# Kernel tuning notes

Hardware: AMD Instinct MI355X
Metric: run time of the kernel (lower is better)

Reference implementation:

```python
import jax, jax.numpy as jnp
import numpy as np

B, D, T, H, OUT = 256, 256, 256, 512, 256

def setup_inputs() -> dict:
    key = jax.random.key(0)
    ks = jax.random.split(key, 7)
    s = lambda fan: 1.0 / np.sqrt(fan)
    x = jax.random.normal(ks[0], (B, D, T), dtype=jnp.float32)
    Wx = jax.random.normal(ks[1], (D, H), dtype=jnp.float32) * s(D)
    Wh = jax.random.normal(ks[2], (H, H), dtype=jnp.float32) * s(H)
    b = jnp.zeros((H,), dtype=jnp.float32)
    Wout = jax.random.normal(ks[3], (H, OUT), dtype=jnp.float32) * s(H)
    bout = jnp.zeros((OUT,), dtype=jnp.float32)
    init_state = jnp.zeros((1, H), dtype=jnp.float32)  # non-trainable zeros in keras
    return {"x": x, "Wx": Wx, "Wh": Wh, "b": b, "Wout": Wout, "bout": bout, "init_state": init_state}

def reference(x, Wx, Wh, b, Wout, bout, init_state):
    # x: [B, D, T] (time on last axis, as unstacked in the keras layer)
    batch = x.shape[0]
    h0 = jnp.tile(init_state, (batch, 1))              # [B, H]
    xs = jnp.moveaxis(x, -1, 0)                        # [T, B, D]
    # precompute input projections for all steps (hoisted out of the recurrence)
    xproj = jnp.einsum('tbd,dh->tbh', xs, Wx) + b      # [T, B, H]

    def step(h_prev, xp):
        cur = jnp.tanh(xp + h_prev @ Wh)
        # residual: state_i = cell_out + state_{i-1}; at i=0 h_prev is zeros, so always adding is exact
        new = cur + h_prev
        return new, new

    _, states = jax.lax.scan(step, h0, xproj)          # states: [T, B, H]
    states = jnp.moveaxis(states, 0, 1)                # [B, T, H]
    out = states @ Wout + bout                         # [B, T, OUT]
    return out
```

## Files before the change

### kernel.cpp

```cpp
#include <hip/hip_runtime.h>
#include <cstring>
#include <cstdio>

typedef __attribute__((ext_vector_type(8))) short short8;
typedef __attribute__((ext_vector_type(4))) float f32x4;
typedef __attribute__((ext_vector_type(4))) unsigned u32x4;

__device__ __forceinline__ short f2bf(float f){
  unsigned u; __builtin_memcpy(&u, &f, 4);
  u += 0x7FFFu + ((u >> 16) & 1u);
  return (short)(u >> 16);
}
__device__ __forceinline__ float bf2f(short s){
  unsigned u = ((unsigned)(unsigned short)s) << 16;
  float f; __builtin_memcpy(&f, &u, 4);
  return f;
}
__device__ __forceinline__ void split2(float v, short& hi, short& lo){
  hi = f2bf(v);
  float r = v - bf2f(hi);
  lo = f2bf(r);
}
__device__ __forceinline__ unsigned pack2(float v){
  short hi, lo; split2(v, hi, lo);
  return (((unsigned)(unsigned short)hi) << 16) | (unsigned)(unsigned short)lo;
}
__device__ __forceinline__ float tanh_fast(float x){
  float e = __expf(2.0f * x);
  return 1.0f - 2.0f / (e + 1.0f);
}

#define HIDX(r,k) ((((r) * 512) + (k)) ^ (((r) & 7) << 3))

__global__ void transpose_split(const float* __restrict__ in,
                                short* __restrict__ outh, short* __restrict__ outl,
                                int R, int C){
  int idx = blockIdx.x * 256 + threadIdx.x;
  if (idx < R * C){
    int r = idx / C, c = idx % C;
    short h, l; split2(in[(size_t)r * C + c], h, l);
    outh[(size_t)c * R + r] = h;
    outl[(size_t)c * R + r] = l;
  }
}

__global__ void transpose_to_bf16(const float* __restrict__ in, short* __restrict__ out,
                                  int R, int C){
  int idx = blockIdx.x * 256 + threadIdx.x;
  if (idx < R * C){
    int r = idx / C, c = idx % C;
    out[(size_t)c * R + r] = f2bf(in[(size_t)r * C + c]);
  }
}

__global__ __launch_bounds__(256) void transpose_x_split(const float* __restrict__ x,
                                                         short* __restrict__ xTh,
                                                         short* __restrict__ xTl){
  __shared__ float tile[64][65];
  const int b = blockIdx.x, d0 = blockIdx.y * 64, t0 = blockIdx.z * 64;
  const int tid = threadIdx.x;
  const float* xp = x + ((size_t)b * 256 + d0) * 256 + t0;
  for (int v = tid; v < 1024; v += 256){
    int r = v >> 4, c4 = (v & 15) * 4;
    float4 f = *(const float4*)(xp + (size_t)r * 256 + c4);
    tile[r][c4+0] = f.x; tile[r][c4+1] = f.y; tile[r][c4+2] = f.z; tile[r][c4+3] = f.w;
  }
  __syncthreads();
  for (int v = tid; v < 512; v += 256){
    int j = v >> 3, i8 = (v & 7) * 8;
    short8 oh, ol;
    #pragma unroll
    for (int u = 0; u < 8; ++u){ short h, l; split2(tile[i8 + u][j], h, l); oh[u] = h; ol[u] = l; }
    size_t off = ((size_t)(t0 + j) * 256 + b) * 256 + d0 + i8;
    *(short8*)(xTh + off) = oh;
    *(short8*)(xTl + off) = ol;
  }
}

__global__ __launch_bounds__(256) void gemm1_split(
    const short* __restrict__ Ah, const short* __restrict__ Al,
    const short* __restrict__ Bh, const short* __restrict__ Bl,
    const float* __restrict__ bias, float* __restrict__ C0, float* __restrict__ C1,
    int M, int N, int K)
{
  __shared__ short lAh[128][72];
  __shared__ short lAl[128][72];
  __shared__ short lBh[128][72];
  __shared__ short lBl[128][72];
  const int m0 = blockIdx.y * 128, n0 = blockIdx.x * 128;
  const int tid = threadIdx.x;
  const int lane = tid & 63, wave = tid >> 6;
  const int wm = (wave >> 1) * 64, wn = (wave & 1) * 64;
  f32x4 acc[4][4] = {};
  for (int k0 = 0; k0 < K; k0 += 64){
    __syncthreads();
    for (int v = tid; v < 4096; v += 256){
      int sel = v >> 10, idx = v & 1023;
      int r = idx >> 3, c = (idx & 7) * 8;
      const short* src = (sel == 0) ? Ah + (size_t)(m0 + r) * K + k0 + c
                       : (sel == 1) ? Al + (size_t)(m0 + r) * K + k0 + c
                       : (sel == 2) ? Bh + (size_t)(n0 + r) * K + k0 + c
                                    : Bl + (size_t)(n0 + r) * K + k0 + c;
      short8 val = *(const short8*)src;
      short* dst = (sel == 0) ? &lAh[r][c] : (sel == 1) ? &lAl[r][c]
                 : (sel == 2) ? &lBh[r][c] : &lBl[r][c];
      *(short8*)dst = val;
    }
    __syncthreads();
    #pragma unroll
    for (int kk = 0; kk < 64; kk += 32){
      int ko = kk + (lane >> 4) * 8;
      short8 ah[4], al[4], bh[4], bl[4];
      #pragma unroll
      for (int i = 0; i < 4; ++i){
        ah[i] = *(const short8*)&lAh[wm + i * 16 + (lane & 15)][ko];
        al[i] = *(const short8*)&lAl[wm + i * 16 + (lane & 15)][ko];
        bh[i] = *(const short8*)&lBh[wn + i * 16 + (lane & 15)][ko];
        bl[i] = *(const short8*)&lBl[wn + i * 16 + (lane & 15)][ko];
      }
      #pragma unroll
      for (int i = 0; i < 4; ++i)
      #pragma unroll
      for (int j = 0; j < 4; ++j){
        acc[i][j] = __builtin_amdgcn_mfma_f32_16x16x32_bf16(ah[i], bh[j], acc[i][j], 0, 0, 0);
        acc[i][j] = __builtin_amdgcn_mfma_f32_16x16x32_bf16(ah[i], bl[j], acc[i][j], 0, 0, 0);
        acc[i][j] = __builtin_amdgcn_mfma_f32_16x16x32_bf16(al[i], bh[j], acc[i][j], 0, 0, 0);
      }
    }
  }
  const int cr = (lane >> 4) * 4, cc = lane & 15;
  #pragma unroll
  for (int i = 0; i < 4; ++i)
  #pragma unroll
  for (int j = 0; j < 4; ++j){
    int row = m0 + wm + i * 16 + cr;
    int col = n0 + wn + j * 16 + cc;
    float bv = bias[col];
    float* base = (row < 32768) ? C0 : C1;
    int rr = (row < 32768) ? row : row - 32768;
    #pragma unroll
    for (int r = 0; r < 4; ++r){
      base[(size_t)(rr + r) * N + col] = acc[i][j][r] + bv;
    }
  }
}

__global__ __launch_bounds__(256, 1) void rnn_steps_v7(
    const float* __restrict__ xp0,
    const float* __restrict__ xp1,
    const short* __restrict__ WhTh,
    const short* __restrict__ WhTl,
    const float* __restrict__ init,
    short* __restrict__ states,
    unsigned* __restrict__ pay,
    unsigned* __restrict__ flags)
{
  __shared__ short hh[16 * 512];
  __shared__ short hl[16 * 512];
  const int tid = threadIdx.x, lane = tid & 63, wave = tid >> 6;
  const int team = blockIdx.x & 31, slice = blockIdx.x >> 5;
  const int b0 = team * 8;
  const int nc = slice * 64 + wave * 16;

  short8 Bh[16], Bl[16];
  {
    const size_t col = (size_t)(nc + (lane & 15));
    const int kb0 = (lane >> 4) * 8;
    #pragma unroll
    for (int ks = 0; ks < 16; ++ks){
      Bh[ks] = *(const short8*)(WhTh + col * 512 + ks * 32 + kb0);
      Bl[ks] = *(const short8*)(WhTl + col * 512 + ks * 32 + kb0);
    }
    #pragma unroll
    for (int ks = 0; ks < 16; ++ks){
      asm volatile("" : "+v"(Bh[ks]), "+v"(Bl[ks]));
    }
  }
  for (int v = tid; v < 8 * 512; v += 256){
    int r = 8 + (v >> 9), k = v & 511;
    hh[HIDX(r, k)] = 0; hl[HIDX(r, k)] = 0;
  }
  for (int v = tid; v < 8 * 512; v += 256){
    int r = v >> 9, k = v & 511;
    short hi, lo; split2(init[k], hi, lo);
    hh[HIDX(r, k)] = hi; hl[HIDX(r, k)] = lo;
  }
  __syncthreads();

  const int cc = lane & 15;
  const bool islo = (lane < 32);
  const int mbase = ((lane & 31) >> 4) * 4;
  const int m_0 = mbase + (islo ? 0 : 2);
  const int m_1 = mbase + (islo ? 1 : 3);
  const int n = nc + cc;
  float hr0 = init[n], hr1 = init[n];

  const int am = lane & 15, kb = (lane >> 4) * 8;
  const int rr = tid & 7, c0 = ((tid >> 3) & 31) * 16;

  for (int t = 0; t < 256; ++t){
    float xv0, xv1;
    if (t == 0){
      xv0 = xp0[(size_t)(b0 + m_0) * 512 + n];
      xv1 = xp0[(size_t)(b0 + m_1) * 512 + n];
    } else {
      const unsigned tagv = (unsigned)t;
      const unsigned* flg = flags + (((size_t)(t & 1)) * 32 + team) * 32 + (lane & 7) * 4;
      while (true){
        u32x4 f;
        asm volatile("global_load_dwordx4 %0, %1, off sc0 sc1" : "=&v"(f) : "v"(flg) : "memory");
        asm volatile("s_waitcnt vmcnt(0)" : "+v"(f) :: "memory");
        bool ok = (f.x >= tagv) && (f.y >= tagv) && (f.z >= tagv) && (f.w >= tagv);
        if (__all(ok)) break;
      }
      const unsigned* src = pay + ((((size_t)(t & 1)) * 32 + team) * 8 + rr) * 512 + c0;
      u32x4 g0, g1, g2, g3;
      asm volatile("global_load_dwordx4 %0, %1, off sc0 sc1" : "=&v"(g0) : "v"(src +  0) : "memory");
      asm volatile("global_load_dwordx4 %0, %1, off sc0 sc1" : "=&v"(g1) : "v"(src +  4) : "memory");
      asm volatile("global_load_dwordx4 %0, %1, off sc0 sc1" : "=&v"(g2) : "v"(src +  8) : "memory");
      asm volatile("global_load_dwordx4 %0, %1, off sc0 sc1" : "=&v"(g3) : "v"(src + 12) : "memory");
      const float* xpb = (t < 128) ? xp0 : xp1;
      const int tt = (t < 128) ? t : t - 128;
      const float* xa0 = xpb + ((size_t)tt * 256 + b0 + m_0) * 512 + n;
      const float* xa1 = xpb + ((size_t)tt * 256 + b0 + m_1) * 512 + n;
      asm volatile("global_load_dword %0, %1, off" : "=&v"(xv0) : "v"(xa0) : "memory");
      asm volatile("global_load_dword %0, %1, off" : "=&v"(xv1) : "v"(xa1) : "memory");
      __syncthreads();
      asm volatile("s_waitcnt vmcnt(2)"
                   : "+v"(g0), "+v"(g1), "+v"(g2), "+v"(g3) :: "memory");
      short8 h0v, h1v, l0v, l1v;
      h0v[0] = (short)(g0.x >> 16); h0v[1] = (short)(g0.y >> 16);
      h0v[2] = (short)(g0.z >> 16); h0v[3] = (short)(g0.w >> 16);
      h0v[4] = (short)(g1.x >> 16); h0v[5] = (short)(g1.y >> 16);
      h0v[6] = (short)(g1.z >> 16); h0v[7] = (short)(g1.w >> 16);
      h1v[0] = (short)(g2.x >> 16); h1v[1] = (short)(g2.y >> 16);
      h1v[2] = (short)(g2.z >> 16); h1v[3] = (short)(g2.w >> 16);
      h1v[4] = (short)(g3.x >> 16); h1v[5] = (short)(g3.y >> 16);
      h1v[6] = (short)(g3.z >> 16); h1v[7] = (short)(g3.w >> 16);
      l0v[0] = (short)(g0.x & 0xffffu); l0v[1] = (short)(g0.y & 0xffffu);
      l0v[2] = (short)(g0.z & 0xffffu); l0v[3] = (short)(g0.w & 0xffffu);
      l0v[4] = (short)(g1.x & 0xffffu); l0v[5] = (short)(g1.y & 0xffffu);
      l0v[6] = (short)(g1.z & 0xffffu); l0v[7] = (short)(g1.w & 0xffffu);
      l1v[0] = (short)(g2.x & 0xffffu); l1v[1] = (short)(g2.y & 0xffffu);
      l1v[2] = (short)(g2.z & 0xffffu); l1v[3] = (short)(g2.w & 0xffffu);
      l1v[4] = (short)(g3.x & 0xffffu); l1v[5] = (short)(g3.y & 0xffffu);
      l1v[6] = (short)(g3.z & 0xffffu); l1v[7] = (short)(g3.w & 0xffffu);
      *(short8*)&hh[HIDX(rr, c0)]     = h0v;
      *(short8*)&hh[HIDX(rr, c0 + 8)] = h1v;
      *(short8*)&hl[HIDX(rr, c0)]     = l0v;
      *(short8*)&hl[HIDX(rr, c0 + 8)] = l1v;
      __syncthreads();
    }

    f32x4 ahh = {}, ahl = {}, alh = {};
    #pragma unroll
    for (int ks = 0; ks < 16; ++ks){
      short8 Ah = *(const short8*)&hh[HIDX(am, ks * 32 + kb)];
      short8 Al = *(const short8*)&hl[HIDX(am, ks * 32 + kb)];
      ahh = __builtin_amdgcn_mfma_f32_16x16x32_bf16(Ah, Bh[ks], ahh, 0, 0, 0);
      ahl = __builtin_amdgcn_mfma_f32_16x16x32_bf16(Ah, Bl[ks], ahl, 0, 0, 0);
      alh = __builtin_amdgcn_mfma_f32_16x16x32_bf16(Al, Bh[ks], alh, 0, 0, 0);
    }
    const float s0 = ahh[0] + (ahl[0] + alh[0]);
    const float s1 = ahh[1] + (ahl[1] + alh[1]);
    const float s2 = ahh[2] + (ahl[2] + alh[2]);
    const float s3 = ahh[3] + (ahl[3] + alh[3]);
    const float t2 = __shfl(s2, lane ^ 32);
    const float t3 = __shfl(s3, lane ^ 32);
    const float v0 = islo ? s0 : t2;
    const float v1 = islo ? s1 : t3;

    if (t > 0){
      asm volatile("s_waitcnt vmcnt(0)" : "+v"(xv0), "+v"(xv1) :: "memory");
    }
    const float hn0 = tanh_fast(xv0 + v0) + hr0;
    const float hn1 = tanh_fast(xv1 + v1) + hr1;
    hr0 = hn0; hr1 = hn1;

    if (t < 255){
      unsigned* dst = pay + ((((size_t)((t + 1) & 1)) * 32 + team) * 8) * 512;
      unsigned w0 = pack2(hn0), w1 = pack2(hn1);
      unsigned* a0 = dst + (size_t)m_0 * 512 + n;
      unsigned* a1 = dst + (size_t)m_1 * 512 + n;
      asm volatile("global_store_dword %0, %1, off sc0 sc1" :: "v"(a0), "v"(w0) : "memory");
      asm volatile("global_store_dword %0, %1, off sc0 sc1" :: "v"(a1), "v"(w1) : "memory");
      asm volatile("s_waitcnt vmcnt(0)" ::: "memory");
      if (lane == 0){
        unsigned* fdst = flags + (((size_t)((t + 1) & 1)) * 32 + team) * 32 + slice * 4 + wave;
        unsigned tagn = (unsigned)(t + 1);
        asm volatile("global_store_dword %0, %1, off sc0 sc1" :: "v"(fdst), "v"(tagn) : "memory");
      }
    }
    states[((size_t)(b0 + m_0) * 256 + t) * 512 + n] = f2bf(hn0);
    states[((size_t)(b0 + m_1) * 256 + t) * 512 + n] = f2bf(hn1);
  }
}

__global__ __launch_bounds__(256) void gemm_bias_f32(
    const short* __restrict__ A, const short* __restrict__ Bt,
    const float* __restrict__ bias, float* __restrict__ C,
    int M, int N, int K)
{
  __shared__ short lA[128][72];
  __shared__ short lB[128][72];
  const int m0 = blockIdx.y * 128, n0 = blockIdx.x * 128;
  const int tid = threadIdx.x;
  const int lane = tid & 63, wave = tid >> 6;
  const int wm = (wave >> 1) * 64, wn = (wave & 1) * 64;
  f32x4 acc[4][4] = {};
  for (int k0 = 0; k0 < K; k0 += 64){
    __syncthreads();
    for (int v = tid; v < 2048; v += 256){
      int sel = v >> 10, idx = v & 1023;
      int r = idx >> 3, c = (idx & 7) * 8;
      const short* src = (sel == 0) ? A + (size_t)(m0 + r) * K + k0 + c
                                    : Bt + (size_t)(n0 + r) * K + k0 + c;
      short8 val = *(const short8*)src;
      short* dst = (sel == 0) ? &lA[r][c] : &lB[r][c];
      *(short8*)dst = val;
    }
    __syncthreads();
    #pragma unroll
    for (int kk = 0; kk < 64; kk += 32){
      int ko = kk + (lane >> 4) * 8;
      short8 a[4], b[4];
      #pragma unroll
      for (int i = 0; i < 4; ++i){
        a[i] = *(const short8*)&lA[wm + i * 16 + (lane & 15)][ko];
        b[i] = *(const short8*)&lB[wn + i * 16 + (lane & 15)][ko];
      }
      #pragma unroll
      for (int i = 0; i < 4; ++i)
      #pragma unroll
      for (int j = 0; j < 4; ++j){
        acc[i][j] = __builtin_amdgcn_mfma_f32_16x16x32_bf16(a[i], b[j], acc[i][j], 0, 0, 0);
      }
    }
  }
  const int cr = (lane >> 4) * 4, cc = lane & 15;
  #pragma unroll
  for (int i = 0; i < 4; ++i)
  #pragma unroll
  for (int j = 0; j < 4; ++j){
    int row = m0 + wm + i * 16 + cr;
    int col = n0 + wn + j * 16 + cc;
    float bv = bias[col];
    #pragma unroll
    for (int r = 0; r < 4; ++r){
      C[(size_t)(row + r) * N + col] = acc[i][j][r] + bv;
    }
  }
}

extern "C" void kernel_launch(void* const* d_in, const int* in_sizes, int n_in,
                              void* d_out, int out_size, void* d_ws, size_t ws_size,
                              hipStream_t stream){
  (void)in_sizes; (void)n_in; (void)out_size;
  const float* x    = (const float*)d_in[0];
  const float* Wx   = (const float*)d_in[1];
  const float* Wh   = (const float*)d_in[2];
  const float* bias = (const float*)d_in[3];
  const float* Wout = (const float*)d_in[4];
  const float* bout = (const float*)d_in[5];
  const float* init = (const float*)d_in[6];
  float* out = (float*)d_out;

  char* p = (char*)d_ws;
  short* xTh    = (short*)(p);
  short* xTl    = (short*)(p + 33554432);
  short* states = (short*)(p);
  float* xproj0 = (float*)(p + 67108864);
  float* xproj1 = (float*)d_out;
  short* WxTh   = (short*)(p + 134217728);
  short* WxTl   = (short*)(p + 134479872);
  short* WhTh   = (short*)(p + 134742016);
  short* WhTl   = (short*)(p + 135266304);
  short* WoutT  = (short*)(p + 135790592);
  unsigned* pay   = (unsigned*)(p + 136052736);
  unsigned* flags = (unsigned*)(p + 137101312);
  if (ws_size < 137109504u){
    fprintf(stderr, "kernel_launch: ws_size=%zu < 137109504 needed\n", ws_size);
  }

  hipMemsetAsync(flags, 0, 8192, stream);

  transpose_split<<<(256*512 + 255)/256, 256, 0, stream>>>(Wx, WxTh, WxTl, 256, 512);
  transpose_split<<<(512*512 + 255)/256, 256, 0, stream>>>(Wh, WhTh, WhTl, 512, 512);
  transpose_to_bf16<<<(512*256 + 255)/256, 256, 0, stream>>>(Wout, WoutT, 512, 256);
  transpose_x_split<<<dim3(256, 4, 4), 256, 0, stream>>>(x, xTh, xTl);
  gemm1_split<<<dim3(4, 512), 256, 0, stream>>>(xTh, xTl, WxTh, WxTl, bias,
                                                xproj0, xproj1, 65536, 512, 256);
  rnn_steps_v7<<<256, 256, 0, stream>>>(xproj0, xproj1, WhTh, WhTl, init,
                                        states, pay, flags);
  gemm_bias_f32<<<dim3(2, 512), 256, 0, stream>>>(states, WoutT, bout, out, 65536, 256, 512);
}
```

Measured before the change: 1.004 ms.

## Interleave two independent batch groups per block in RNN recurrence kernel

The recurrence kernel now launches 128 blocks instead of 256. Each block handles two 8-row batch groups with separate LDS buffers and flag sets, alternating between them every timestep so that waiting on one group's cross-block flags can overlap with compute on the other. The spin loop gains an s_sleep, and the states store is moved ahead of the vmcnt wait before the flag is published. The trade-off is half as many CUs in use and twice the serial work per block, in exchange for hiding inter-block synchronization latency.

```diff
diff --git a/kernel.cpp b/kernel.cpp
--- a/kernel.cpp
+++ b/kernel.cpp
@@ -145,7 +145,7 @@
   }
 }
 
-__global__ __launch_bounds__(256, 1) void rnn_steps_v7(
+__global__ __launch_bounds__(256, 1) void rnn_steps_v8(
     const float* __restrict__ xp0,
     const float* __restrict__ xp1,
     const short* __restrict__ WhTh,
@@ -155,11 +155,12 @@
     unsigned* __restrict__ pay,
     unsigned* __restrict__ flags)
 {
-  __shared__ short hh[16 * 512];
-  __shared__ short hl[16 * 512];
+  __shared__ short hhA[16 * 512];
+  __shared__ short hlA[16 * 512];
+  __shared__ short hhB[16 * 512];
+  __shared__ short hlB[16 * 512];
   const int tid = threadIdx.x, lane = tid & 63, wave = tid >> 6;
-  const int team = blockIdx.x & 31, slice = blockIdx.x >> 5;
-  const int b0 = team * 8;
+  const int team = blockIdx.x & 15, slice = blockIdx.x >> 4;
   const int nc = slice * 64 + wave * 16;
 
   short8 Bh[16], Bl[16];
@@ -178,12 +179,14 @@
   }
   for (int v = tid; v < 8 * 512; v += 256){
     int r = 8 + (v >> 9), k = v & 511;
-    hh[HIDX(r, k)] = 0; hl[HIDX(r, k)] = 0;
+    hhA[HIDX(r, k)] = 0; hlA[HIDX(r, k)] = 0;
+    hhB[HIDX(r, k)] = 0; hlB[HIDX(r, k)] = 0;
   }
   for (int v = tid; v < 8 * 512; v += 256){
     int r = v >> 9, k = v & 511;
     short hi, lo; split2(init[k], hi, lo);
-    hh[HIDX(r, k)] = hi; hl[HIDX(r, k)] = lo;
+    hhA[HIDX(r, k)] = hi; hlA[HIDX(r, k)] = lo;
+    hhB[HIDX(r, k)] = hi; hlB[HIDX(r, k)] = lo;
   }
   __syncthreads();
 
@@ -193,106 +196,122 @@
   const int m_0 = mbase + (islo ? 0 : 2);
   const int m_1 = mbase + (islo ? 1 : 3);
   const int n = nc + cc;
-  float hr0 = init[n], hr1 = init[n];
+  float hrA0 = init[n], hrA1 = init[n];
+  float hrB0 = init[n], hrB1 = init[n];
 
   const int am = lane & 15, kb = (lane >> 4) * 8;
   const int rr = tid & 7, c0 = ((tid >> 3) & 31) * 16;
 
   for (int t = 0; t < 256; ++t){
-    float xv0, xv1;
-    if (t == 0){
-      xv0 = xp0[(size_t)(b0 + m_0) * 512 + n];
-      xv1 = xp0[(size_t)(b0 + m_1) * 512 + n];
-    } else {
-      const unsigned tagv = (unsigned)t;
-      const unsigned* flg = flags + (((size_t)(t & 1)) * 32 + team) * 32 + (lane & 7) * 4;
-      while (true){
-        u32x4 f;
-        asm volatile("global_load_dwordx4 %0, %1, off sc0 sc1" : "=&v"(f) : "v"(flg) : "memory");
-        asm volatile("s_waitcnt vmcnt(0)" : "+v"(f) :: "memory");
-        bool ok = (f.x >= tagv) && (f.y >= tagv) && (f.z >= tagv) && (f.w >= tagv);
-        if (__all(ok)) break;
-      }
-      const unsigned* src = pay + ((((size_t)(t & 1)) * 32 + team) * 8 + rr) * 512 + c0;
-      u32x4 g0, g1, g2, g3;
-      asm volatile("global_load_dwordx4 %0, %1, off sc0 sc1" : "=&v"(g0) : "v"(src +  0) : "memory");
-      asm volatile("global_load_dwordx4 %0, %1, off sc0 sc1" : "=&v"(g1) : "v"(src +  4) : "memory");
-      asm volatile("global_load_dwordx4 %0, %1, off sc0 sc1" : "=&v"(g2) : "v"(src +  8) : "memory");
-      asm volatile("global_load_dwordx4 %0, %1, off sc0 sc1" : "=&v"(g3) : "v"(src + 12) : "memory");
-      const float* xpb = (t < 128) ? xp0 : xp1;
-      const int tt = (t < 128) ? t : t - 128;
-      const float* xa0 = xpb + ((size_t)tt * 256 + b0 + m_0) * 512 + n;
-      const float* xa1 = xpb + ((size_t)tt * 256 + b0 + m_1) * 512 + n;
-      asm volatile("global_load_dword %0, %1, off" : "=&v"(xv0) : "v"(xa0) : "memory");
-      asm volatile("global_load_dword %0, %1, off" : "=&v"(xv1) : "v"(xa1) : "memory");
-      __syncthreads();
-      asm volatile("s_waitcnt vmcnt(2)"
-                   : "+v"(g0), "+v"(g1), "+v"(g2), "+v"(g3) :: "memory");
-      short8 h0v, h1v, l0v, l1v;
-      h0v[0] = (short)(g0.x >> 16); h0v[1] = (short)(g0.y >> 16);
-      h0v[2] = (short)(g0.z >> 16); h0v[3] = (short)(g0.w >> 16);
-      h0v[4] = (short)(g1.x >> 16); h0v[5] = (short)(g1.y >> 16);
-      h0v[6] = (short)(g1.z >> 16); h0v[7] = (short)(g1.w >> 16);
-      h1v[0] = (short)(g2.x >> 16); h1v[1] = (short)(g2.y >> 16);
-      h1v[2] = (short)(g2.z >> 16); h1v[3] = (short)(g2.w >> 16);
-      h1v[4] = (short)(g3.x >> 16); h1v[5] = (short)(g3.y >> 16);
-      h1v[6] = (short)(g3.z >> 16); h1v[7] = (short)(g3.w >> 16);
-      l0v[0] = (short)(g0.x & 0xffffu); l0v[1] = (short)(g0.y & 0xffffu);
-      l0v[2] = (short)(g0.z & 0xffffu); l0v[3] = (short)(g0.w & 0xffffu);
-      l0v[4] = (short)(g1.x & 0xffffu); l0v[5] = (short)(g1.y & 0xffffu);
-      l0v[6] = (short)(g1.z & 0xffffu); l0v[7] = (short)(g1.w & 0xffffu);
-      l1v[0] = (short)(g2.x & 0xffffu); l1v[1] = (short)(g2.y & 0xffffu);
-      l1v[2] = (short)(g2.z & 0xffffu); l1v[3] = (short)(g2.w & 0xffffu);
-      l1v[4] = (short)(g3.x & 0xffffu); l1v[5] = (short)(g3.y & 0xffffu);
-      l1v[6] = (short)(g3.z & 0xffffu); l1v[7] = (short)(g3.w & 0xffffu);
-      *(short8*)&hh[HIDX(rr, c0)]     = h0v;
-      *(short8*)&hh[HIDX(rr, c0 + 8)] = h1v;
-      *(short8*)&hl[HIDX(rr, c0)]     = l0v;
-      *(short8*)&hl[HIDX(rr, c0 + 8)] = l1v;
-      __syncthreads();
-    }
-
-    f32x4 ahh = {}, ahl = {}, alh = {};
-    #pragma unroll
-    for (int ks = 0; ks < 16; ++ks){
-      short8 Ah = *(const short8*)&hh[HIDX(am, ks * 32 + kb)];
-      short8 Al = *(const short8*)&hl[HIDX(am, ks * 32 + kb)];
-      ahh = __builtin_amdgcn_mfma_f32_16x16x32_bf16(Ah, Bh[ks], ahh, 0, 0, 0);
-      ahl = __builtin_amdgcn_mfma_f32_16x16x32_bf16(Ah, Bl[ks], ahl, 0, 0, 0);
-      alh = __builtin_amdgcn_mfma_f32_16x16x32_bf16(Al, Bh[ks], alh, 0, 0, 0);
-    }
-    const float s0 = ahh[0] + (ahl[0] + alh[0]);
-    const float s1 = ahh[1] + (ahl[1] + alh[1]);
-    const float s2 = ahh[2] + (ahl[2] + alh[2]);
-    const float s3 = ahh[3] + (ahl[3] + alh[3]);
-    const float t2 = __shfl(s2, lane ^ 32);
-    const float t3 = __shfl(s3, lane ^ 32);
-    const float v0 = islo ? s0 : t2;
-    const float v1 = islo ? s1 : t3;
-
-    if (t > 0){
-      asm volatile("s_waitcnt vmcnt(0)" : "+v"(xv0), "+v"(xv1) :: "memory");
-    }
-    const float hn0 = tanh_fast(xv0 + v0) + hr0;
-    const float hn1 = tanh_fast(xv1 + v1) + hr1;
-    hr0 = hn0; hr1 = hn1;
-
-    if (t < 255){
-      unsigned* dst = pay + ((((size_t)((t + 1) & 1)) * 32 + team) * 8) * 512;
-      unsigned w0 = pack2(hn0), w1 = pack2(hn1);
-      unsigned* a0 = dst + (size_t)m_0 * 512 + n;
-      unsigned* a1 = dst + (size_t)m_1 * 512 + n;
-      asm volatile("global_store_dword %0, %1, off sc0 sc1" :: "v"(a0), "v"(w0) : "memory");
-      asm volatile("global_store_dword %0, %1, off sc0 sc1" :: "v"(a1), "v"(w1) : "memory");
-      asm volatile("s_waitcnt vmcnt(0)" ::: "memory");
-      if (lane == 0){
-        unsigned* fdst = flags + (((size_t)((t + 1) & 1)) * 32 + team) * 32 + slice * 4 + wave;
-        unsigned tagn = (unsigned)(t + 1);
-        asm volatile("global_store_dword %0, %1, off sc0 sc1" :: "v"(fdst), "v"(tagn) : "memory");
-      }
-    }
-    states[((size_t)(b0 + m_0) * 256 + t) * 512 + n] = f2bf(hn0);
-    states[((size_t)(b0 + m_1) * 256 + t) * 512 + n] = f2bf(hn1);
+    #pragma unroll
+    for (int g = 0; g < 2; ++g){
+      short* hh = (g == 0) ? hhA : hhB;
+      short* hl = (g == 0) ? hlA : hlB;
+      float& hr0 = (g == 0) ? hrA0 : hrB0;
+      float& hr1 = (g == 0) ? hrA1 : hrB1;
+      const int b0g = team * 16 + g * 8;
+
+      float xv0, xv1;
+      if (t == 0){
+        xv0 = xp0[(size_t)(b0g + m_0) * 512 + n];
+        xv1 = xp0[(size_t)(b0g + m_1) * 512 + n];
+      } else {
+        const unsigned tagv = (unsigned)t;
+        const unsigned* flg = flags + ((((size_t)(t & 1)) * 2 + g) * 16 + team) * 32
+                              + (lane & 7) * 4;
+        while (true){
+          u32x4 f;
+          asm volatile("global_load_dwordx4 %0, %1, off sc0 sc1" : "=&v"(f) : "v"(flg) : "memory");
+          asm volatile("s_waitcnt vmcnt(0)" : "+v"(f) :: "memory");
+          bool ok = (f.x >= tagv) && (f.y >= tagv) && (f.z >= tagv) && (f.w >= tagv);
+          if (__all(ok)) break;
+          __builtin_amdgcn_s_sleep(1);
+        }
+        const unsigned* src = pay + ((((size_t)(t & 1)) * 16 + team) * 16 + g * 8 + rr) * 512 + c0;
+        u32x4 g0, g1, g2, g3;
+        asm volatile("global_load_dwordx4 %0, %1, off sc0 sc1" : "=&v"(g0) : "v"(src +  0) : "memory");
+        asm volatile("global_load_dwordx4 %0, %1, off sc0 sc1" : "=&v"(g1) : "v"(src +  4) : "memory");
+        asm volatile("global_load_dwordx4 %0, %1, off sc0 sc1" : "=&v"(g2) : "v"(src +  8) : "memory");
+        asm volatile("global_load_dwordx4 %0, %1, off sc0 sc1" : "=&v"(g3) : "v"(src + 12) : "memory");
+        const float* xpb = (t < 128) ? xp0 : xp1;
+        const int tt = (t < 128) ? t : t - 128;
+        const float* xa0 = xpb + ((size_t)tt * 256 + b0g + m_0) * 512 + n;
+        const float* xa1 = xpb + ((size_t)tt * 256 + b0g + m_1) * 512 + n;
+        asm volatile("global_load_dword %0, %1, off" : "=&v"(xv0) : "v"(xa0) : "memory");
+        asm volatile("global_load_dword %0, %1, off" : "=&v"(xv1) : "v"(xa1) : "memory");
+        __syncthreads();
+        asm volatile("s_waitcnt vmcnt(2)"
+                     : "+v"(g0), "+v"(g1), "+v"(g2), "+v"(g3) :: "memory");
+        short8 h0v, h1v, l0v, l1v;
+        h0v[0] = (short)(g0.x >> 16); h0v[1] = (short)(g0.y >> 16);
+        h0v[2] = (short)(g0.z >> 16); h0v[3] = (short)(g0.w >> 16);
+        h0v[4] = (short)(g1.x >> 16); h0v[5] = (short)(g1.y >> 16);
+        h0v[6] = (short)(g1.z >> 16); h0v[7] = (short)(g1.w >> 16);
+        h1v[0] = (short)(g2.x >> 16); h1v[1] = (short)(g2.y >> 16);
+        h1v[2] = (short)(g2.z >> 16); h1v[3] = (short)(g2.w >> 16);
+        h1v[4] = (short)(g3.x >> 16); h1v[5] = (short)(g3.y >> 16);
+        h1v[6] = (short)(g3.z >> 16); h1v[7] = (short)(g3.w >> 16);
+        l0v[0] = (short)(g0.x & 0xffffu); l0v[1] = (short)(g0.y & 0xffffu);
+        l0v[2] = (short)(g0.z & 0xffffu); l0v[3] = (short)(g0.w & 0xffffu);
+        l0v[4] = (short)(g1.x & 0xffffu); l0v[5] = (short)(g1.y & 0xffffu);
+        l0v[6] = (short)(g1.z & 0xffffu); l0v[7] = (short)(g1.w & 0xffffu);
+        l1v[0] = (short)(g2.x & 0xffffu); l1v[1] = (short)(g2.y & 0xffffu);
+        l1v[2] = (short)(g2.z & 0xffffu); l1v[3] = (short)(g2.w & 0xffffu);
+        l1v[4] = (short)(g3.x & 0xffffu); l1v[5] = (short)(g3.y & 0xffffu);
+        l1v[6] = (short)(g3.z & 0xffffu); l1v[7] = (short)(g3.w & 0xffffu);
+        *(short8*)&hh[HIDX(rr, c0)]     = h0v;
+        *(short8*)&hh[HIDX(rr, c0 + 8)] = h1v;
+        *(short8*)&hl[HIDX(rr, c0)]     = l0v;
+        *(short8*)&hl[HIDX(rr, c0 + 8)] = l1v;
+        __syncthreads();
+      }
+
+      f32x4 ahh = {}, ahl = {}, alh = {};
+      #pragma unroll
+      for (int ks = 0; ks < 16; ++ks){
+        short8 Ah = *(const short8*)&hh[HIDX(am, ks * 32 + kb)];
+        short8 Al = *(const short8*)&hl[HIDX(am, ks * 32 + kb)];
+        ahh = __builtin_amdgcn_mfma_f32_16x16x32_bf16(Ah, Bh[ks], ahh, 0, 0, 0);
+        ahl = __builtin_amdgcn_mfma_f32_16x16x32_bf16(Ah, Bl[ks], ahl, 0, 0, 0);
+        alh = __builtin_amdgcn_mfma_f32_16x16x32_bf16(Al, Bh[ks], alh, 0, 0, 0);
+      }
+      const float s0 = ahh[0] + (ahl[0] + alh[0]);
+      const float s1 = ahh[1] + (ahl[1] + alh[1]);
+      const float s2 = ahh[2] + (ahl[2] + alh[2]);
+      const float s3 = ahh[3] + (ahl[3] + alh[3]);
+      const float t2 = __shfl(s2, lane ^ 32);
+      const float t3 = __shfl(s3, lane ^ 32);
+      const float v0 = islo ? s0 : t2;
+      const float v1 = islo ? s1 : t3;
+
+      if (t > 0){
+        asm volatile("s_waitcnt vmcnt(0)" : "+v"(xv0), "+v"(xv1) :: "memory");
+      }
+      const float hn0 = tanh_fast(xv0 + v0) + hr0;
+      const float hn1 = tanh_fast(xv1 + v1) + hr1;
+      hr0 = hn0; hr1 = hn1;
+
+      if (t < 255){
+        unsigned* dst = pay + ((((size_t)((t + 1) & 1)) * 16 + team) * 16 + g * 8) * 512;
+        unsigned w0 = pack2(hn0), w1 = pack2(hn1);
+        unsigned* a0 = dst + (size_t)m_0 * 512 + n;
+        unsigned* a1 = dst + (size_t)m_1 * 512 + n;
+        asm volatile("global_store_dword %0, %1, off sc0 sc1" :: "v"(a0), "v"(w0) : "memory");
+        asm volatile("global_store_dword %0, %1, off sc0 sc1" :: "v"(a1), "v"(w1) : "memory");
+        states[((size_t)(b0g + m_0) * 256 + t) * 512 + n] = f2bf(hn0);
+        states[((size_t)(b0g + m_1) * 256 + t) * 512 + n] = f2bf(hn1);
+        asm volatile("s_waitcnt vmcnt(0)" ::: "memory");
+        if (lane == 0){
+          unsigned* fdst = flags + ((((size_t)((t + 1) & 1)) * 2 + g) * 16 + team) * 32
+                           + slice * 4 + wave;
+          unsigned tagn = (unsigned)(t + 1);
+          asm volatile("global_store_dword %0, %1, off sc0 sc1" :: "v"(fdst), "v"(tagn) : "memory");
+        }
+      } else {
+        states[((size_t)(b0g + m_0) * 256 + t) * 512 + n] = f2bf(hn0);
+        states[((size_t)(b0g + m_1) * 256 + t) * 512 + n] = f2bf(hn1);
+      }
+    }
   }
 }
 
@@ -390,7 +409,7 @@
   transpose_x_split<<<dim3(256, 4, 4), 256, 0, stream>>>(x, xTh, xTl);
   gemm1_split<<<dim3(4, 512), 256, 0, stream>>>(xTh, xTl, WxTh, WxTl, bias,
                                                 xproj0, xproj1, 65536, 512, 256);
-  rnn_steps_v7<<<256, 256, 0, stream>>>(xproj0, xproj1, WhTh, WhTl, init,
+  rnn_steps_v8<<<128, 256, 0, stream>>>(xproj0, xproj1, WhTh, WhTl, init,
                                         states, pay, flags);
   gemm_bias_f32<<<dim3(2, 512), 256, 0, stream>>>(states, WoutT, bout, out, 65536, 256, 512);
 }
```

Measured after the change: 1.515 ms. 50.9% more time.

## Use one flag per block with prefetched flag reads in RNN step sync

Applied to the files above, without the earlier changes.

The cross-block handshake in the recurrent kernel changes from one flag per wave to one flag per block. Each block raises its flag once after a block barrier, which now sits after the payload stores instead of after the payload loads. Flags for the next step are prefetched right after publishing, so the spin loop, which now sleeps between polls, is only entered if the prefetched values are stale. The block skips its own flag, and the state stores move before the barrier. The intent is fewer polling loads and less sync latency on the serial step chain. The risk is memory-ordering bugs: the hidden-state LDS buffers may be overwritten while other waves still read them, now that the barrier after the loads is gone.

```diff
diff --git a/kernel.cpp b/kernel.cpp
--- a/kernel.cpp
+++ b/kernel.cpp
@@ -145,7 +145,7 @@
   }
 }
 
-__global__ __launch_bounds__(256, 1) void rnn_steps_v7(
+__global__ __launch_bounds__(256, 1) void rnn_steps_v9(
     const float* __restrict__ xp0,
     const float* __restrict__ xp1,
     const short* __restrict__ WhTh,
@@ -198,6 +198,8 @@
   const int am = lane & 15, kb = (lane >> 4) * 8;
   const int rr = tid & 7, c0 = ((tid >> 3) & 31) * 16;
 
+  u32x4 pf0 = {}, pf1 = {};
+
   for (int t = 0; t < 256; ++t){
     float xv0, xv1;
     if (t == 0){
@@ -205,13 +207,24 @@
       xv1 = xp0[(size_t)(b0 + m_1) * 512 + n];
     } else {
       const unsigned tagv = (unsigned)t;
-      const unsigned* flg = flags + (((size_t)(t & 1)) * 32 + team) * 32 + (lane & 7) * 4;
-      while (true){
-        u32x4 f;
-        asm volatile("global_load_dwordx4 %0, %1, off sc0 sc1" : "=&v"(f) : "v"(flg) : "memory");
-        asm volatile("s_waitcnt vmcnt(0)" : "+v"(f) :: "memory");
-        bool ok = (f.x >= tagv) && (f.y >= tagv) && (f.z >= tagv) && (f.w >= tagv);
-        if (__all(ok)) break;
+      bool ok = (pf0.x >= tagv || slice == 0) && (pf0.y >= tagv || slice == 1) &&
+                (pf0.z >= tagv || slice == 2) && (pf0.w >= tagv || slice == 3) &&
+                (pf1.x >= tagv || slice == 4) && (pf1.y >= tagv || slice == 5) &&
+                (pf1.z >= tagv || slice == 6) && (pf1.w >= tagv || slice == 7);
+      if (!ok){
+        const unsigned* flg = flags + (((size_t)(t & 1)) * 32 + team) * 32;
+        while (true){
+          __builtin_amdgcn_s_sleep(1);
+          u32x4 f0, f1;
+          asm volatile("global_load_dwordx4 %0, %1, off sc0 sc1" : "=&v"(f0) : "v"(flg)     : "memory");
+          asm volatile("global_load_dwordx4 %0, %1, off sc0 sc1" : "=&v"(f1) : "v"(flg + 4) : "memory");
+          asm volatile("s_waitcnt vmcnt(0)" : "+v"(f0), "+v"(f1) :: "memory");
+          bool ok2 = (f0.x >= tagv || slice == 0) && (f0.y >= tagv || slice == 1) &&
+                     (f0.z >= tagv || slice == 2) && (f0.w >= tagv || slice == 3) &&
+                     (f1.x >= tagv || slice == 4) && (f1.y >= tagv || slice == 5) &&
+                     (f1.z >= tagv || slice == 6) && (f1.w >= tagv || slice == 7);
+          if (ok2) break;
+        }
       }
       const unsigned* src = pay + ((((size_t)(t & 1)) * 32 + team) * 8 + rr) * 512 + c0;
       u32x4 g0, g1, g2, g3;
@@ -225,7 +238,6 @@
       const float* xa1 = xpb + ((size_t)tt * 256 + b0 + m_1) * 512 + n;
       asm volatile("global_load_dword %0, %1, off" : "=&v"(xv0) : "v"(xa0) : "memory");
       asm volatile("global_load_dword %0, %1, off" : "=&v"(xv1) : "v"(xa1) : "memory");
-      __syncthreads();
       asm volatile("s_waitcnt vmcnt(2)"
                    : "+v"(g0), "+v"(g1), "+v"(g2), "+v"(g3) :: "memory");
       short8 h0v, h1v, l0v, l1v;
@@ -284,15 +296,22 @@
       unsigned* a1 = dst + (size_t)m_1 * 512 + n;
       asm volatile("global_store_dword %0, %1, off sc0 sc1" :: "v"(a0), "v"(w0) : "memory");
       asm volatile("global_store_dword %0, %1, off sc0 sc1" :: "v"(a1), "v"(w1) : "memory");
-      asm volatile("s_waitcnt vmcnt(0)" ::: "memory");
-      if (lane == 0){
-        unsigned* fdst = flags + (((size_t)((t + 1) & 1)) * 32 + team) * 32 + slice * 4 + wave;
+      states[((size_t)(b0 + m_0) * 256 + t) * 512 + n] = f2bf(hn0);
+      states[((size_t)(b0 + m_1) * 256 + t) * 512 + n] = f2bf(hn1);
+      const unsigned* nflg = flags + (((size_t)((t + 1) & 1)) * 32 + team) * 32;
+      asm volatile("global_load_dwordx4 %0, %1, off sc0 sc1" : "=&v"(pf0) : "v"(nflg)     : "memory");
+      asm volatile("global_load_dwordx4 %0, %1, off sc0 sc1" : "=&v"(pf1) : "v"(nflg + 4) : "memory");
+      asm volatile("s_waitcnt vmcnt(0)" : "+v"(pf0), "+v"(pf1) :: "memory");
+      __syncthreads();
+      if (tid == 0){
+        unsigned* fdst = flags + (((size_t)((t + 1) & 1)) * 32 + team) * 32 + slice;
         unsigned tagn = (unsigned)(t + 1);
         asm volatile("global_store_dword %0, %1, off sc0 sc1" :: "v"(fdst), "v"(tagn) : "memory");
       }
-    }
-    states[((size_t)(b0 + m_0) * 256 + t) * 512 + n] = f2bf(hn0);
-    states[((size_t)(b0 + m_1) * 256 + t) * 512 + n] = f2bf(hn1);
+    } else {
+      states[((size_t)(b0 + m_0) * 256 + t) * 512 + n] = f2bf(hn0);
+      states[((size_t)(b0 + m_1) * 256 + t) * 512 + n] = f2bf(hn1);
+    }
   }
 }
 
@@ -390,7 +409,7 @@
   transpose_x_split<<<dim3(256, 4, 4), 256, 0, stream>>>(x, xTh, xTl);
   gemm1_split<<<dim3(4, 512), 256, 0, stream>>>(xTh, xTl, WxTh, WxTl, bias,
                                                 xproj0, xproj1, 65536, 512, 256);
-  rnn_steps_v7<<<256, 256, 0, stream>>>(xproj0, xproj1, WhTh, WhTl, init,
+  rnn_steps_v9<<<256, 256, 0, stream>>>(xproj0, xproj1, WhTh, WhTl, init,
                                         states, pay, flags);
   gemm_bias_f32<<<dim3(2, 512), 256, 0, stream>>>(states, WoutT, bout, out, 65536, 256, 512);
 }
```

Measured after the change: 977.9 us. -2.6%, faster.

## Use 16-row batch teams in persistent RNN, halving blocks and fusing flag signals

Applied to the files above, without the earlier changes.

The recurrent kernel now runs 16 teams of 16 batch rows each on 128 blocks, where it previously ran 32 teams of 8 rows on 256 blocks. Each MFMA tile is fully used, so the cross-lane shuffle and the zero-padding rows go away. Each block now publishes one flag per step after a block barrier instead of one per wave. The spin-wait reads 8 flags with a short sleep between polls. This cuts wasted MFMA work and inter-block sync traffic per step, in exchange for half as many CUs doing the serial recurrence and an extra barrier before signalling.

```diff
diff --git a/kernel.cpp b/kernel.cpp
--- a/kernel.cpp
+++ b/kernel.cpp
@@ -145,7 +145,7 @@
   }
 }
 
-__global__ __launch_bounds__(256, 1) void rnn_steps_v7(
+__global__ __launch_bounds__(256, 1) void rnn_steps_v10(
     const float* __restrict__ xp0,
     const float* __restrict__ xp1,
     const short* __restrict__ WhTh,
@@ -158,8 +158,8 @@
   __shared__ short hh[16 * 512];
   __shared__ short hl[16 * 512];
   const int tid = threadIdx.x, lane = tid & 63, wave = tid >> 6;
-  const int team = blockIdx.x & 31, slice = blockIdx.x >> 5;
-  const int b0 = team * 8;
+  const int team = blockIdx.x & 15, slice = blockIdx.x >> 4;
+  const int b0 = team * 16;
   const int nc = slice * 64 + wave * 16;
 
   short8 Bh[16], Bl[16];
@@ -176,80 +176,81 @@
       asm volatile("" : "+v"(Bh[ks]), "+v"(Bl[ks]));
     }
   }
-  for (int v = tid; v < 8 * 512; v += 256){
-    int r = 8 + (v >> 9), k = v & 511;
-    hh[HIDX(r, k)] = 0; hl[HIDX(r, k)] = 0;
-  }
-  for (int v = tid; v < 8 * 512; v += 256){
+  for (int v = tid; v < 16 * 512; v += 256){
     int r = v >> 9, k = v & 511;
     short hi, lo; split2(init[k], hi, lo);
     hh[HIDX(r, k)] = hi; hl[HIDX(r, k)] = lo;
   }
   __syncthreads();
 
-  const int cc = lane & 15;
-  const bool islo = (lane < 32);
-  const int mbase = ((lane & 31) >> 4) * 4;
-  const int m_0 = mbase + (islo ? 0 : 2);
-  const int m_1 = mbase + (islo ? 1 : 3);
-  const int n = nc + cc;
-  float hr0 = init[n], hr1 = init[n];
+  const int n = nc + (lane & 15);
+  const int mrow = (lane >> 4) * 4;
+  float hr0 = init[n], hr1 = init[n], hr2 = init[n], hr3 = init[n];
 
   const int am = lane & 15, kb = (lane >> 4) * 8;
-  const int rr = tid & 7, c0 = ((tid >> 3) & 31) * 16;
+  const int rr = tid & 15, c0 = (tid >> 4) * 32;
 
   for (int t = 0; t < 256; ++t){
-    float xv0, xv1;
+    float xv0, xv1, xv2, xv3;
     if (t == 0){
-      xv0 = xp0[(size_t)(b0 + m_0) * 512 + n];
-      xv1 = xp0[(size_t)(b0 + m_1) * 512 + n];
+      xv0 = xp0[(size_t)(b0 + mrow + 0) * 512 + n];
+      xv1 = xp0[(size_t)(b0 + mrow + 1) * 512 + n];
+      xv2 = xp0[(size_t)(b0 + mrow + 2) * 512 + n];
+      xv3 = xp0[(size_t)(b0 + mrow + 3) * 512 + n];
     } else {
       const unsigned tagv = (unsigned)t;
-      const unsigned* flg = flags + (((size_t)(t & 1)) * 32 + team) * 32 + (lane & 7) * 4;
+      const unsigned* flg = flags + (((size_t)(t & 1)) * 16 + team) * 32;
       while (true){
-        u32x4 f;
-        asm volatile("global_load_dwordx4 %0, %1, off sc0 sc1" : "=&v"(f) : "v"(flg) : "memory");
-        asm volatile("s_waitcnt vmcnt(0)" : "+v"(f) :: "memory");
-        bool ok = (f.x >= tagv) && (f.y >= tagv) && (f.z >= tagv) && (f.w >= tagv);
-        if (__all(ok)) break;
-      }
-      const unsigned* src = pay + ((((size_t)(t & 1)) * 32 + team) * 8 + rr) * 512 + c0;
-      u32x4 g0, g1, g2, g3;
+        u32x4 f0, f1;
+        asm volatile("global_load_dwordx4 %0, %1, off sc0 sc1" : "=&v"(f0) : "v"(flg)     : "memory");
+        asm volatile("global_load_dwordx4 %0, %1, off sc0 sc1" : "=&v"(f1) : "v"(flg + 4) : "memory");
+        asm volatile("s_waitcnt vmcnt(0)" : "+v"(f0), "+v"(f1) :: "memory");
+        if (f0.x >= tagv && f0.y >= tagv && f0.z >= tagv && f0.w >= tagv &&
+            f1.x >= tagv && f1.y >= tagv && f1.z >= tagv && f1.w >= tagv) break;
+        __builtin_amdgcn_s_sleep(1);
+      }
+      const unsigned* src = pay + ((((size_t)(t & 1)) * 16 + team) * 16 + rr) * 512 + c0;
+      u32x4 g0, g1, g2, g3, g4, g5, g6, g7;
       asm volatile("global_load_dwordx4 %0, %1, off sc0 sc1" : "=&v"(g0) : "v"(src +  0) : "memory");
       asm volatile("global_load_dwordx4 %0, %1, off sc0 sc1" : "=&v"(g1) : "v"(src +  4) : "memory");
       asm volatile("global_load_dwordx4 %0, %1, off sc0 sc1" : "=&v"(g2) : "v"(src +  8) : "memory");
       asm volatile("global_load_dwordx4 %0, %1, off sc0 sc1" : "=&v"(g3) : "v"(src + 12) : "memory");
+      asm volatile("global_load_dwordx4 %0, %1, off sc0 sc1" : "=&v"(g4) : "v"(src + 16) : "memory");
+      asm volatile("global_load_dwordx4 %0, %1, off sc0 sc1" : "=&v"(g5) : "v"(src + 20) : "memory");
+      asm volatile("global_load_dwordx4 %0, %1, off sc0 sc1" : "=&v"(g6) : "v"(src + 24) : "memory");
+      asm volatile("global_load_dwordx4 %0, %1, off sc0 sc1" : "=&v"(g7) : "v"(src + 28) : "memory");
       const float* xpb = (t < 128) ? xp0 : xp1;
       const int tt = (t < 128) ? t : t - 128;
-      const float* xa0 = xpb + ((size_t)tt * 256 + b0 + m_0) * 512 + n;
-      const float* xa1 = xpb + ((size_t)tt * 256 + b0 + m_1) * 512 + n;
-      asm volatile("global_load_dword %0, %1, off" : "=&v"(xv0) : "v"(xa0) : "memory");
-      asm volatile("global_load_dword %0, %1, off" : "=&v"(xv1) : "v"(xa1) : "memory");
-      __syncthreads();
-      asm volatile("s_waitcnt vmcnt(2)"
-                   : "+v"(g0), "+v"(g1), "+v"(g2), "+v"(g3) :: "memory");
-      short8 h0v, h1v, l0v, l1v;
-      h0v[0] = (short)(g0.x >> 16); h0v[1] = (short)(g0.y >> 16);
-      h0v[2] = (short)(g0.z >> 16); h0v[3] = (short)(g0.w >> 16);
-      h0v[4] = (short)(g1.x >> 16); h0v[5] = (short)(g1.y >> 16);
-      h0v[6] = (short)(g1.z >> 16); h0v[7] = (short)(g1.w >> 16);
-      h1v[0] = (short)(g2.x >> 16); h1v[1] = (short)(g2.y >> 16);
-      h1v[2] = (short)(g2.z >> 16); h1v[3] = (short)(g2.w >> 16);
-      h1v[4] = (short)(g3.x >> 16); h1v[5] = (short)(g3.y >> 16);
-      h1v[6] = (short)(g3.z >> 16); h1v[7] = (short)(g3.w >> 16);
-      l0v[0] = (short)(g0.x & 0xffffu); l0v[1] = (short)(g0.y & 0xffffu);
-      l0v[2] = (short)(g0.z & 0xffffu); l0v[3] = (short)(g0.w & 0xffffu);
-      l0v[4] = (short)(g1.x & 0xffffu); l0v[5] = (short)(g1.y & 0xffffu);
-      l0v[6] = (short)(g1.z & 0xffffu); l0v[7] = (short)(g1.w & 0xffffu);
-      l1v[0] = (short)(g2.x & 0xffffu); l1v[1] = (short)(g2.y & 0xffffu);
-      l1v[2] = (short)(g2.z & 0xffffu); l1v[3] = (short)(g2.w & 0xffffu);
-      l1v[4] = (short)(g3.x & 0xffffu); l1v[5] = (short)(g3.y & 0xffffu);
-      l1v[6] = (short)(g3.z & 0xffffu); l1v[7] = (short)(g3.w & 0xffffu);
-      *(short8*)&hh[HIDX(rr, c0)]     = h0v;
-      *(short8*)&hh[HIDX(rr, c0 + 8)] = h1v;
-      *(short8*)&hl[HIDX(rr, c0)]     = l0v;
-      *(short8*)&hl[HIDX(rr, c0 + 8)] = l1v;
-      __syncthreads();
+      const float* xa = xpb + ((size_t)tt * 256 + b0 + mrow) * 512 + n;
+      asm volatile("global_load_dword %0, %1, off" : "=&v"(xv0) : "v"(xa)        : "memory");
+      asm volatile("global_load_dword %0, %1, off" : "=&v"(xv1) : "v"(xa +  512) : "memory");
+      asm volatile("global_load_dword %0, %1, off" : "=&v"(xv2) : "v"(xa + 1024) : "memory");
+      asm volatile("global_load_dword %0, %1, off" : "=&v"(xv3) : "v"(xa + 1536) : "memory");
+      asm volatile("s_waitcnt vmcnt(4)"
+                   : "+v"(g0), "+v"(g1), "+v"(g2), "+v"(g3),
+                     "+v"(g4), "+v"(g5), "+v"(g6), "+v"(g7) :: "memory");
+      #define UNPK(gA, gB, OFF)                                            \
+      {                                                                    \
+        short8 hv, lv;                                                     \
+        hv[0] = (short)(gA.x >> 16); hv[1] = (short)(gA.y >> 16);          \
+        hv[2] = (short)(gA.z >> 16); hv[3] = (short)(gA.w >> 16);          \
+        hv[4] = (short)(gB.x >> 16); hv[5] = (short)(gB.y >> 16);          \
+        hv[6] = (short)(gB.z >> 16); hv[7] = (short)(gB.w >> 16);          \
+        lv[0] = (short)(gA.x & 0xffffu); lv[1] = (short)(gA.y & 0xffffu);  \
+        lv[2] = (short)(gA.z & 0xffffu); lv[3] = (short)(gA.w & 0xffffu);  \
+        lv[4] = (short)(gB.x & 0xffffu); lv[5] = (short)(gB.y & 0xffffu);  \
+        lv[6] = (short)(gB.z & 0xffffu); lv[7] = (short)(gB.w & 0xffffu);  \
+        *(short8*)&hh[HIDX(rr, c0 + OFF)] = hv;                            \
+        *(short8*)&hl[HIDX(rr, c0 + OFF)] = lv;                            \
+      }
+      UNPK(g0, g1, 0)
+      UNPK(g2, g3, 8)
+      UNPK(g4, g5, 16)
+      UNPK(g6, g7, 24)
+      #undef UNPK
+      asm volatile("s_waitcnt lgkmcnt(0)" ::: "memory");
+      __builtin_amdgcn_s_barrier();
+      __builtin_amdgcn_sched_barrier(0);
     }
 
     f32x4 ahh = {}, ahl = {}, alh = {};
@@ -265,34 +266,40 @@
     const float s1 = ahh[1] + (ahl[1] + alh[1]);
     const float s2 = ahh[2] + (ahl[2] + alh[2]);
     const float s3 = ahh[3] + (ahl[3] + alh[3]);
-    const float t2 = __shfl(s2, lane ^ 32);
-    const float t3 = __shfl(s3, lane ^ 32);
-    const float v0 = islo ? s0 : t2;
-    const float v1 = islo ? s1 : t3;
 
     if (t > 0){
-      asm volatile("s_waitcnt vmcnt(0)" : "+v"(xv0), "+v"(xv1) :: "memory");
-    }
-    const float hn0 = tanh_fast(xv0 + v0) + hr0;
-    const float hn1 = tanh_fast(xv1 + v1) + hr1;
-    hr0 = hn0; hr1 = hn1;
+      asm volatile("s_waitcnt vmcnt(0)"
+                   : "+v"(xv0), "+v"(xv1), "+v"(xv2), "+v"(xv3) :: "memory");
+    }
+    const float hn0 = tanh_fast(xv0 + s0) + hr0;
+    const float hn1 = tanh_fast(xv1 + s1) + hr1;
+    const float hn2 = tanh_fast(xv2 + s2) + hr2;
+    const float hn3 = tanh_fast(xv3 + s3) + hr3;
+    hr0 = hn0; hr1 = hn1; hr2 = hn2; hr3 = hn3;
 
     if (t < 255){
-      unsigned* dst = pay + ((((size_t)((t + 1) & 1)) * 32 + team) * 8) * 512;
-      unsigned w0 = pack2(hn0), w1 = pack2(hn1);
-      unsigned* a0 = dst + (size_t)m_0 * 512 + n;
-      unsigned* a1 = dst + (size_t)m_1 * 512 + n;
+      unsigned* dst = pay + ((((size_t)((t + 1) & 1)) * 16 + team) * 16) * 512;
+      unsigned w0 = pack2(hn0), w1 = pack2(hn1), w2 = pack2(hn2), w3 = pack2(hn3);
+      unsigned* a0 = dst + (size_t)(mrow + 0) * 512 + n;
+      unsigned* a1 = dst + (size_t)(mrow + 1) * 512 + n;
+      unsigned* a2 = dst + (size_t)(mrow + 2) * 512 + n;
+      unsigned* a3 = dst + (size_t)(mrow + 3) * 512 + n;
       asm volatile("global_store_dword %0, %1, off sc0 sc1" :: "v"(a0), "v"(w0) : "memory");
       asm volatile("global_store_dword %0, %1, off sc0 sc1" :: "v"(a1), "v"(w1) : "memory");
+      asm volatile("global_store_dword %0, %1, off sc0 sc1" :: "v"(a2), "v"(w2) : "memory");
+      asm volatile("global_store_dword %0, %1, off sc0 sc1" :: "v"(a3), "v"(w3) : "memory");
       asm volatile("s_waitcnt vmcnt(0)" ::: "memory");
-      if (lane == 0){
-        unsigned* fdst = flags + (((size_t)((t + 1) & 1)) * 32 + team) * 32 + slice * 4 + wave;
+      __syncthreads();
+      if (tid == 0){
+        unsigned* fdst = flags + (((size_t)((t + 1) & 1)) * 16 + team) * 32 + slice;
         unsigned tagn = (unsigned)(t + 1);
         asm volatile("global_store_dword %0, %1, off sc0 sc1" :: "v"(fdst), "v"(tagn) : "memory");
       }
     }
-    states[((size_t)(b0 + m_0) * 256 + t) * 512 + n] = f2bf(hn0);
-    states[((size_t)(b0 + m_1) * 256 + t) * 512 + n] = f2bf(hn1);
+    states[((size_t)(b0 + mrow + 0) * 256 + t) * 512 + n] = f2bf(hn0);
+    states[((size_t)(b0 + mrow + 1) * 256 + t) * 512 + n] = f2bf(hn1);
+    states[((size_t)(b0 + mrow + 2) * 256 + t) * 512 + n] = f2bf(hn2);
+    states[((size_t)(b0 + mrow + 3) * 256 + t) * 512 + n] = f2bf(hn3);
   }
 }
 
@@ -378,11 +385,11 @@
   short* WoutT  = (short*)(p + 135790592);
   unsigned* pay   = (unsigned*)(p + 136052736);
   unsigned* flags = (unsigned*)(p + 137101312);
-  if (ws_size < 137109504u){
-    fprintf(stderr, "kernel_launch: ws_size=%zu < 137109504 needed\n", ws_size);
-  }
-
-  hipMemsetAsync(flags, 0, 8192, stream);
+  if (ws_size < 137105408u){
+    fprintf(stderr, "kernel_launch: ws_size=%zu < 137105408 needed\n", ws_size);
+  }
+
+  hipMemsetAsync(flags, 0, 4096, stream);
 
   transpose_split<<<(256*512 + 255)/256, 256, 0, stream>>>(Wx, WxTh, WxTl, 256, 512);
   transpose_split<<<(512*512 + 255)/256, 256, 0, stream>>>(Wh, WhTh, WhTl, 512, 512);
@@ -390,7 +397,7 @@
   transpose_x_split<<<dim3(256, 4, 4), 256, 0, stream>>>(x, xTh, xTl);
   gemm1_split<<<dim3(4, 512), 256, 0, stream>>>(xTh, xTl, WxTh, WxTl, bias,
                                                 xproj0, xproj1, 65536, 512, 256);
-  rnn_steps_v7<<<256, 256, 0, stream>>>(xproj0, xproj1, WhTh, WhTl, init,
-                                        states, pay, flags);
+  rnn_steps_v10<<<128, 256, 0, stream>>>(xproj0, xproj1, WhTh, WhTl, init,
+                                         states, pay, flags);
   gemm_bias_f32<<<dim3(2, 512), 256, 0, stream>>>(states, WoutT, bout, out, 65536, 256, 512);
 }
```

Result: slower. 1.252 ms (+24.7%).
